# Kernel tuning notes

Hardware: AMD Instinct MI355X
Metric: run time of the kernel (lower is better)

Reference implementation:

```python
import jax, jax.numpy as jnp
import numpy as np
import math

D_MODEL = 1024
N_HEAD = 16


def setup_inputs() -> dict:
    key = jax.random.key(0)
    ks = jax.random.split(key, 5)
    x = jax.random.normal(ks[0], (2, 2048, D_MODEL), dtype=jnp.float32)
    # Linear params (torch Linear: y = x @ W.T + b); store as [in, out] for einsum
    s1 = 1.0 / math.sqrt(D_MODEL)
    W_qkv = jax.random.uniform(ks[1], (D_MODEL, 3 * D_MODEL), jnp.float32, -s1, s1)
    b_qkv = jax.random.uniform(ks[2], (3 * D_MODEL,), jnp.float32, -s1, s1)
    W_out = jax.random.uniform(ks[3], (D_MODEL, D_MODEL), jnp.float32, -s1, s1)
    b_out = jax.random.uniform(ks[4], (D_MODEL,), jnp.float32, -s1, s1)
    return {"x": x, "W_qkv": W_qkv, "b_qkv": b_qkv, "W_out": W_out, "b_out": b_out}


def reference(x, W_qkv, b_qkv, W_out, b_out):
    B, L, D = x.shape
    H = N_HEAD
    hd = D // H
    qkv = x @ W_qkv + b_qkv                      # [B, L, 3D]
    q, k, v = jnp.split(qkv, 3, axis=-1)
    # [B, H, L, hd]
    q = q.reshape(B, L, H, hd).transpose(0, 2, 1, 3)
    k = k.reshape(B, L, H, hd).transpose(0, 2, 1, 3)
    v = v.reshape(B, L, H, hd).transpose(0, 2, 1, 3)
    scale = 1.0 / math.sqrt(hd)
    scores = jnp.einsum('bhqd,bhkd->bhqk', q, k) * scale   # [B, H, L, L]
    causal = jnp.tril(jnp.ones((L, L), dtype=bool))
    scores = jnp.where(causal, scores, jnp.float32(-jnp.inf))
    probs = jax.nn.softmax(scores, axis=-1)
    out = jnp.einsum('bhqk,bhkd->bhqd', probs, v)          # [B, H, L, hd]
    out = out.transpose(0, 2, 1, 3).reshape(B, L, D)
    out = out @ W_out + b_out
    return jnp.squeeze(out)
```

## Files before the change

### kernel.cpp

```cpp
#include <hip/hip_runtime.h>
#include <hip/hip_bf16.h>

#define SEQ    2048
#define NHEAD  16
#define HD     64
#define DMODEL 1024

using bf16 = __hip_bfloat16;
using short8 = __attribute__((ext_vector_type(8))) short;
using short4v = __attribute__((ext_vector_type(4))) short;
using f32x4  = __attribute__((ext_vector_type(4))) float;

__device__ __forceinline__ float fast_exp2(float x) {
  return __builtin_amdgcn_exp2f(x);
}
#define WAIT_LGKM0() __builtin_amdgcn_s_waitcnt(0xC07F)

__device__ __forceinline__ void gload_lds16(const bf16* g, bf16* l) {
  __builtin_amdgcn_global_load_lds(
      (const __attribute__((address_space(1))) void*)g,
      (__attribute__((address_space(3))) void*)l, 16, 0, 0);
}


__global__ void prep_k(const float* __restrict__ x, bf16* __restrict__ xb,
                       const float* __restrict__ Wqkv, bf16* __restrict__ WqkvT,
                       const float* __restrict__ Wout, bf16* __restrict__ WoutT) {
  __shared__ bf16 tile[32][33];
  const int id = blockIdx.x, tid = threadIdx.x;
  if (id < 2048) {
    int i = (id * 256 + tid) * 8;
    bf16 tmp[8];
    #pragma unroll
    for (int j = 0; j < 8; ++j) tmp[j] = __float2bfloat16(x[i + j]);
    *(short8*)&xb[i] = *(short8*)tmp;
    return;
  }
  const float* in; bf16* out; int R, C, tx32, ty32;
  if (id < 2048 + 3072) {
    int t = id - 2048; in = Wqkv; out = WqkvT; R = 1024; C = 3072;
    tx32 = t % 96; ty32 = t / 96;
  } else {
    int t = id - 5120; in = Wout; out = WoutT; R = 1024; C = 1024;
    tx32 = t % 32; ty32 = t / 32;
  }
  int c0 = tx32 * 32, r0 = ty32 * 32;
  int tx = tid & 31, ty = tid >> 5;
  #pragma unroll
  for (int i = ty; i < 32; i += 8)
    tile[i][tx] = __float2bfloat16(in[(size_t)(r0 + i) * C + c0 + tx]);
  __syncthreads();
  #pragma unroll
  for (int i = ty; i < 32; i += 8)
    out[(size_t)(c0 + i) * R + r0 + tx] = tile[tx][i];
}

__global__ void transpose_v_k(const bf16* __restrict__ in, bf16* __restrict__ out) {
  __shared__ bf16 tile[32][33];
  const int bh = blockIdx.z;
  const bf16* ip = in  + (size_t)bh * SEQ * HD;
  bf16* op       = out + (size_t)bh * HD * SEQ;
  int c0 = blockIdx.x * 32, r0 = blockIdx.y * 32;
  int tx = threadIdx.x & 31, ty = threadIdx.x >> 5;
  #pragma unroll
  for (int i = ty; i < 32; i += 8)
    tile[i][tx] = ip[(size_t)(r0 + i) * HD + c0 + tx];
  __syncthreads();
  #pragma unroll
  for (int i = ty; i < 32; i += 8)
    op[(size_t)(c0 + i) * SEQ + r0 + tx] = tile[tx][i];
}

template <int MODE>
__global__ __launch_bounds__(256)
void gemm_bt(const bf16* __restrict__ A, const bf16* __restrict__ BT,
             const float* __restrict__ bias,
             bf16* __restrict__ out0, bf16* __restrict__ out1,
             bf16* __restrict__ out2, float* __restrict__ outf) {
  constexpr int K = 1024;
  __shared__ __align__(16) bf16 As[128 * 32];
  __shared__ __align__(16) bf16 Bs[128 * 32];
  const int tid = threadIdx.x;
  const int wave = tid >> 6, lane = tid & 63;
  const int quad = lane >> 4, l16 = lane & 15;
  const int waveM = (wave >> 1) * 64, waveN = (wave & 1) * 64;
  const int m0 = blockIdx.x * 128, n0 = blockIdx.y * 128;
  const int srow = (lane >> 2);
  const int scol = (((lane & 3) ^ ((lane >> 3) & 3)) * 8);
  const int q8   = (quad ^ ((l16 >> 1) & 3)) * 8;

  const f32x4 zero4 = {0.f, 0.f, 0.f, 0.f};
  f32x4 acc[4][4];
  #pragma unroll
  for (int i = 0; i < 4; ++i)
    #pragma unroll
    for (int j = 0; j < 4; ++j) acc[i][j] = zero4;

  for (int k0 = 0; k0 < K; k0 += 32) {
    __syncthreads();
    #pragma unroll
    for (int half = 0; half < 2; ++half) {
      int grow = half * 64 + wave * 16 + srow;
      gload_lds16(&A [(size_t)(m0 + grow) * K + k0 + scol],
                  &As[(half * 64 + wave * 16) * 32]);
      gload_lds16(&BT[(size_t)(n0 + grow) * K + k0 + scol],
                  &Bs[(half * 64 + wave * 16) * 32]);
    }
    __syncthreads();
    short8 af[4], bfm[4];
    #pragma unroll
    for (int mt = 0; mt < 4; ++mt)
      af[mt] = *(const short8*)&As[(waveM + mt * 16 + l16) * 32 + q8];
    #pragma unroll
    for (int nt = 0; nt < 4; ++nt)
      bfm[nt] = *(const short8*)&Bs[(waveN + nt * 16 + l16) * 32 + q8];
    #pragma unroll
    for (int mt = 0; mt < 4; ++mt)
      #pragma unroll
      for (int nt = 0; nt < 4; ++nt)
        acc[mt][nt] = __builtin_amdgcn_mfma_f32_16x16x32_bf16(
            af[mt], bfm[nt], acc[mt][nt], 0, 0, 0);
  }

  #pragma unroll
  for (int nt = 0; nt < 4; ++nt) {
    int n = n0 + waveN + nt * 16 + l16;
    float bvv = bias[n];
    #pragma unroll
    for (int mt = 0; mt < 4; ++mt) {
      #pragma unroll
      for (int r = 0; r < 4; ++r) {
        int m = m0 + waveM + mt * 16 + quad * 4 + r;
        float v = acc[mt][nt][r] + bvv;
        if (MODE == 1) {
          outf[(size_t)m * 1024 + n] = v;
        } else {
          bf16 v16 = __float2bfloat16(v);
          int which = n >> 10, oo = n & 1023;
          int h = oo >> 6, c = oo & 63;
          int b = m >> 11, l = m & 2047;
          size_t idx = ((size_t)(b * NHEAD + h) * SEQ + l) * HD + c;
          if (which == 0)      out0[idx] = v16;
          else if (which == 1) out1[idx] = v16;
          else                 out2[idx] = v16;
        }
      }
    }
  }
}

__global__ __launch_bounds__(256, 2)
void attn_k(const bf16* __restrict__ Q, const bf16* __restrict__ Kb,
            const bf16* __restrict__ VT, bf16* __restrict__ O) {
  __shared__ __align__(16) bf16 Ks[2][2][64 * 32];
  __shared__ __align__(16) bf16 Vs[2][2][64 * 32];
  __shared__ __align__(16) bf16 Plds[4][2][16][72];
  const int tid = threadIdx.x;
  const int wave = tid >> 6, lane = tid & 63;
  const int quad = lane >> 4, l16 = lane & 15;
  const int srow = lane >> 2;
  const int scol = (((lane & 3) ^ ((lane >> 3) & 3)) * 8);
  const int q8   = (quad ^ ((l16 >> 1) & 3)) * 8;
  const int id = blockIdx.x;
  const int bh = id & 31;
  const int qt = 15 - (id >> 5);
  const int b = bh >> 4, h = bh & 15;

  const bf16* Qp = Q  + (size_t)bh * SEQ * HD;
  const bf16* Kp = Kb + (size_t)bh * SEQ * HD;
  const bf16* Vp = VT + (size_t)bh * HD * SEQ;

  const f32x4 zero4 = {0.f, 0.f, 0.f, 0.f};
  const float c = 0.18033688011112042f;
  const float mc = 8.0f * c;

  const int q0w = qt * 128 + wave * 32;
  const int ntiles = 2 * qt + 2;

  short8 qf[2][2];
  #pragma unroll
  for (int g = 0; g < 2; ++g) {
    qf[g][0] = *(const short8*)&Qp[(size_t)(q0w + g * 16 + l16) * HD + quad * 8];
    qf[g][1] = *(const short8*)&Qp[(size_t)(q0w + g * 16 + l16) * HD + 32 + quad * 8];
  }

  f32x4 oacc[2][4];
  #pragma unroll
  for (int g = 0; g < 2; ++g)
    #pragma unroll
    for (int dt = 0; dt < 4; ++dt) oacc[g][dt] = zero4;
  float l4[2][4] = {{0.f, 0.f, 0.f, 0.f}, {0.f, 0.f, 0.f, 0.f}};

  {
    #pragma unroll
    for (int hh = 0; hh < 2; ++hh)
      gload_lds16(&Kp[(size_t)(wave * 16 + srow) * HD + hh * 32 + scol],
                  &Ks[0][hh][(wave * 16) * 32]);
    #pragma unroll
    for (int ch = 0; ch < 2; ++ch)
      gload_lds16(&Vp[(size_t)(wave * 16 + srow) * SEQ + ch * 32 + scol],
                  &Vs[0][ch][(wave * 16) * 32]);
  }
  __syncthreads();

  for (int t = 0; t < ntiles; ++t) {
    const int buf = t & 1;
    if (t + 1 < ntiles) {
      const int k1 = (t + 1) << 6, nb = buf ^ 1;
      #pragma unroll
      for (int hh = 0; hh < 2; ++hh)
        gload_lds16(&Kp[(size_t)(k1 + wave * 16 + srow) * HD + hh * 32 + scol],
                    &Ks[nb][hh][(wave * 16) * 32]);
      #pragma unroll
      for (int ch = 0; ch < 2; ++ch)
        gload_lds16(&Vp[(size_t)(wave * 16 + srow) * SEQ + k1 + ch * 32 + scol],
                    &Vs[nb][ch][(wave * 16) * 32]);
    }
    const int k0 = t << 6;

    f32x4 s[2][4];
    __builtin_amdgcn_s_setprio(1);
    #pragma unroll
    for (int g4 = 0; g4 < 4; ++g4) {
      short8 ka = *(const short8*)&Ks[buf][0][(g4 * 16 + l16) * 32 + q8];
      short8 kb = *(const short8*)&Ks[buf][1][(g4 * 16 + l16) * 32 + q8];
      #pragma unroll
      for (int g = 0; g < 2; ++g) {
        f32x4 sg = zero4;
        sg = __builtin_amdgcn_mfma_f32_16x16x32_bf16(ka, qf[g][0], sg, 0, 0, 0);
        sg = __builtin_amdgcn_mfma_f32_16x16x32_bf16(kb, qf[g][1], sg, 0, 0, 0);
        s[g][g4] = sg;
      }
    }
    __builtin_amdgcn_s_setprio(0);

    if (t >= ntiles - 2) {
      #pragma unroll
      for (int g = 0; g < 2; ++g) {
        const int q_lane = q0w + g * 16 + l16;
        #pragma unroll
        for (int g4 = 0; g4 < 4; ++g4)
          #pragma unroll
          for (int r = 0; r < 4; ++r) {
            int k = k0 + g4 * 16 + quad * 4 + r;
            s[g][g4][r] = (k <= q_lane) ? s[g][g4][r] : -__builtin_inff();
          }
      }
    }

    #pragma unroll
    for (int g = 0; g < 2; ++g)
      #pragma unroll
      for (int g4 = 0; g4 < 4; ++g4) {
        bf16 pb[4];
        #pragma unroll
        for (int r = 0; r < 4; ++r) {
          float p = fast_exp2(__builtin_fmaf(s[g][g4][r], c, -mc));
          l4[g][r] += p;
          pb[r] = __float2bfloat16(p);
        }
        *(short4v*)&Plds[wave][g][l16][g4 * 16 + quad * 4] = *(short4v*)pb;
      }
    WAIT_LGKM0();

    __builtin_amdgcn_s_setprio(1);
    #pragma unroll
    for (int ch = 0; ch < 2; ++ch) {
      short8 pf0 = *(const short8*)&Plds[wave][0][l16][ch * 32 + quad * 8];
      short8 pf1 = *(const short8*)&Plds[wave][1][l16][ch * 32 + quad * 8];
      #pragma unroll
      for (int dt = 0; dt < 4; ++dt) {
        short8 vf = *(const short8*)&Vs[buf][ch][(dt * 16 + l16) * 32 + q8];
        oacc[0][dt] = __builtin_amdgcn_mfma_f32_16x16x32_bf16(vf, pf0, oacc[0][dt], 0, 0, 0);
        oacc[1][dt] = __builtin_amdgcn_mfma_f32_16x16x32_bf16(vf, pf1, oacc[1][dt], 0, 0, 0);
      }
    }
    __builtin_amdgcn_s_setprio(0);
    __syncthreads();
  }

  #pragma unroll
  for (int g = 0; g < 2; ++g) {
    float l_i = (l4[g][0] + l4[g][1]) + (l4[g][2] + l4[g][3]);
    l_i += __shfl_xor(l_i, 16, 64);
    l_i += __shfl_xor(l_i, 32, 64);
    float inv = 1.f / l_i;
    #pragma unroll
    for (int dt = 0; dt < 4; ++dt) {
      bf16 ob[4];
      #pragma unroll
      for (int r = 0; r < 4; ++r) ob[r] = __float2bfloat16(oacc[g][dt][r] * inv);
      *(short4v*)&Plds[wave][g][l16][dt * 16 + quad * 4] = *(short4v*)ob;
    }
  }
  WAIT_LGKM0();
  {
    int row = lane >> 2;
    int col = (lane & 3) * 16;
    #pragma unroll
    for (int g = 0; g < 2; ++g) {
      short8 o0 = *(const short8*)&Plds[wave][g][row][col];
      short8 o1 = *(const short8*)&Plds[wave][g][row][col + 8];
      size_t base =
          ((size_t)(b * SEQ + q0w + g * 16 + row)) * DMODEL + h * HD + col;
      *(short8*)&O[base]     = o0;
      *(short8*)&O[base + 8] = o1;
    }
  }
}

extern "C" void kernel_launch(void* const* d_in, const int* in_sizes, int n_in,
                              void* d_out, int out_size, void* d_ws, size_t ws_size,
                              hipStream_t stream) {
  const float* x    = (const float*)d_in[0];
  const float* Wqkv = (const float*)d_in[1];
  const float* bqkv = (const float*)d_in[2];
  const float* Wout = (const float*)d_in[3];
  const float* bout = (const float*)d_in[4];
  float* out = (float*)d_out;

  char* ws = (char*)d_ws;
  const size_t MB = 1024 * 1024;
  char* big    = ws + 16384;
  bf16* Kbuf   = (bf16*)(big);
  bf16* VTb    = (bf16*)(big + 8 * MB);
  bf16* xb     = (bf16*)(big + 16 * MB);
  bf16* AO     = (bf16*)(big + 16 * MB);
  bf16* WqkvT  = (bf16*)(big + 24 * MB);
  bf16* WoutT  = (bf16*)(big + 30 * MB);
  bf16* Qb     = (bf16*)d_out;
  bf16* Vtmp   = (bf16*)((char*)d_out + 8 * MB);

  prep_k<<<6144, 256, 0, stream>>>(x, xb, Wqkv, WqkvT, Wout, WoutT);
  gemm_bt<0><<<dim3(4096 / 128, 3072 / 128), 256, 0, stream>>>(
      xb, WqkvT, bqkv, Qb, Kbuf, Vtmp, nullptr);
  transpose_v_k<<<dim3(HD / 32, SEQ / 32, 32), 256, 0, stream>>>(Vtmp, VTb);
  attn_k<<<512, 256, 0, stream>>>(Qb, Kbuf, VTb, AO);
  gemm_bt<1><<<dim3(4096 / 128, 1024 / 128), 256, 0, stream>>>(
      AO, WoutT, bout, nullptr, nullptr, nullptr, out);
}
```

Measured before the change: 186.5 us.

## Use 512-thread attention blocks processing paired causal query tiles

The attention kernel now launches 256 blocks of 8 waves, each covering a 256-row query tile, and each block handles two tiles (pairi and 7-pairi) in sequence so every block does the same total causal work. K and V staging is split across waves, with half loading K and half loading V, and the per-wave P scratch grows to 8 waves. This is meant to remove tail imbalance across CUs and halve K/V reloads per query row. In exchange, blocks are larger and the grid is smaller, so fewer waves may be resident per CU, and more tiles need causal masking.

```diff
diff --git a/kernel.cpp b/kernel.cpp
--- a/kernel.cpp
+++ b/kernel.cpp
@@ -149,12 +149,12 @@
   }
 }
 
-__global__ __launch_bounds__(256, 2)
+__global__ __launch_bounds__(512, 2)
 void attn_k(const bf16* __restrict__ Q, const bf16* __restrict__ Kb,
             const bf16* __restrict__ VT, bf16* __restrict__ O) {
   __shared__ __align__(16) bf16 Ks[2][2][64 * 32];
   __shared__ __align__(16) bf16 Vs[2][2][64 * 32];
-  __shared__ __align__(16) bf16 Plds[4][2][16][72];
+  __shared__ __align__(16) bf16 Plds[8][2][16][72];
   const int tid = threadIdx.x;
   const int wave = tid >> 6, lane = tid & 63;
   const int quad = lane >> 4, l16 = lane & 15;
@@ -163,7 +163,7 @@
   const int q8   = (quad ^ ((l16 >> 1) & 3)) * 8;
   const int id = blockIdx.x;
   const int bh = id & 31;
-  const int qt = 15 - (id >> 5);
+  const int pairi = id >> 5;
   const int b = bh >> 4, h = bh & 15;
 
   const bf16* Qp = Q  + (size_t)bh * SEQ * HD;
@@ -174,138 +174,149 @@
   const float c = 0.18033688011112042f;
   const float mc = 8.0f * c;
 
-  const int q0w = qt * 128 + wave * 32;
-  const int ntiles = 2 * qt + 2;
-
-  short8 qf[2][2];
-  #pragma unroll
-  for (int g = 0; g < 2; ++g) {
-    qf[g][0] = *(const short8*)&Qp[(size_t)(q0w + g * 16 + l16) * HD + quad * 8];
-    qf[g][1] = *(const short8*)&Qp[(size_t)(q0w + g * 16 + l16) * HD + 32 + quad * 8];
-  }
-
-  f32x4 oacc[2][4];
-  #pragma unroll
-  for (int g = 0; g < 2; ++g)
-    #pragma unroll
-    for (int dt = 0; dt < 4; ++dt) oacc[g][dt] = zero4;
-  float l4[2][4] = {{0.f, 0.f, 0.f, 0.f}, {0.f, 0.f, 0.f, 0.f}};
-
-  {
-    #pragma unroll
-    for (int hh = 0; hh < 2; ++hh)
-      gload_lds16(&Kp[(size_t)(wave * 16 + srow) * HD + hh * 32 + scol],
-                  &Ks[0][hh][(wave * 16) * 32]);
-    #pragma unroll
-    for (int ch = 0; ch < 2; ++ch)
-      gload_lds16(&Vp[(size_t)(wave * 16 + srow) * SEQ + ch * 32 + scol],
-                  &Vs[0][ch][(wave * 16) * 32]);
-  }
-  __syncthreads();
-
-  for (int t = 0; t < ntiles; ++t) {
-    const int buf = t & 1;
-    if (t + 1 < ntiles) {
-      const int k1 = (t + 1) << 6, nb = buf ^ 1;
-      #pragma unroll
-      for (int hh = 0; hh < 2; ++hh)
-        gload_lds16(&Kp[(size_t)(k1 + wave * 16 + srow) * HD + hh * 32 + scol],
-                    &Ks[nb][hh][(wave * 16) * 32]);
-      #pragma unroll
-      for (int ch = 0; ch < 2; ++ch)
-        gload_lds16(&Vp[(size_t)(wave * 16 + srow) * SEQ + k1 + ch * 32 + scol],
-                    &Vs[nb][ch][(wave * 16) * 32]);
-    }
-    const int k0 = t << 6;
-
-    f32x4 s[2][4];
-    __builtin_amdgcn_s_setprio(1);
-    #pragma unroll
-    for (int g4 = 0; g4 < 4; ++g4) {
-      short8 ka = *(const short8*)&Ks[buf][0][(g4 * 16 + l16) * 32 + q8];
-      short8 kb = *(const short8*)&Ks[buf][1][(g4 * 16 + l16) * 32 + q8];
-      #pragma unroll
-      for (int g = 0; g < 2; ++g) {
-        f32x4 sg = zero4;
-        sg = __builtin_amdgcn_mfma_f32_16x16x32_bf16(ka, qf[g][0], sg, 0, 0, 0);
-        sg = __builtin_amdgcn_mfma_f32_16x16x32_bf16(kb, qf[g][1], sg, 0, 0, 0);
-        s[g][g4] = sg;
-      }
-    }
-    __builtin_amdgcn_s_setprio(0);
-
-    if (t >= ntiles - 2) {
-      #pragma unroll
-      for (int g = 0; g < 2; ++g) {
-        const int q_lane = q0w + g * 16 + l16;
-        #pragma unroll
-        for (int g4 = 0; g4 < 4; ++g4)
+  const int kslab = (wave & 3) * 16;
+  const bool stK = wave < 4;
+
+  for (int pass = 0; pass < 2; ++pass) {
+    const int qt = pass ? (7 - pairi) : pairi;
+    const int q0w = qt * 256 + wave * 32;
+    const int ntiles = 4 * qt + 4;
+
+    short8 qf[2][2];
+    #pragma unroll
+    for (int g = 0; g < 2; ++g) {
+      qf[g][0] = *(const short8*)&Qp[(size_t)(q0w + g * 16 + l16) * HD + quad * 8];
+      qf[g][1] = *(const short8*)&Qp[(size_t)(q0w + g * 16 + l16) * HD + 32 + quad * 8];
+    }
+
+    f32x4 oacc[2][4];
+    #pragma unroll
+    for (int g = 0; g < 2; ++g)
+      #pragma unroll
+      for (int dt = 0; dt < 4; ++dt) oacc[g][dt] = zero4;
+    float l4[2][4] = {{0.f, 0.f, 0.f, 0.f}, {0.f, 0.f, 0.f, 0.f}};
+
+    if (stK) {
+      gload_lds16(&Kp[(size_t)(kslab + srow) * HD + scol],
+                  &Ks[0][0][kslab * 32]);
+      gload_lds16(&Kp[(size_t)(kslab + srow) * HD + 32 + scol],
+                  &Ks[0][1][kslab * 32]);
+    } else {
+      gload_lds16(&Vp[(size_t)(kslab + srow) * SEQ + scol],
+                  &Vs[0][0][kslab * 32]);
+      gload_lds16(&Vp[(size_t)(kslab + srow) * SEQ + 32 + scol],
+                  &Vs[0][1][kslab * 32]);
+    }
+    __syncthreads();
+
+    for (int t = 0; t < ntiles; ++t) {
+      const int buf = t & 1;
+      if (t + 1 < ntiles) {
+        const int k1 = (t + 1) << 6, nb = buf ^ 1;
+        if (stK) {
+          gload_lds16(&Kp[(size_t)(k1 + kslab + srow) * HD + scol],
+                      &Ks[nb][0][kslab * 32]);
+          gload_lds16(&Kp[(size_t)(k1 + kslab + srow) * HD + 32 + scol],
+                      &Ks[nb][1][kslab * 32]);
+        } else {
+          gload_lds16(&Vp[(size_t)(kslab + srow) * SEQ + k1 + scol],
+                      &Vs[nb][0][kslab * 32]);
+          gload_lds16(&Vp[(size_t)(kslab + srow) * SEQ + k1 + 32 + scol],
+                      &Vs[nb][1][kslab * 32]);
+        }
+      }
+      const int k0 = t << 6;
+
+      f32x4 s[2][4];
+      __builtin_amdgcn_s_setprio(1);
+      #pragma unroll
+      for (int g4 = 0; g4 < 4; ++g4) {
+        short8 ka = *(const short8*)&Ks[buf][0][(g4 * 16 + l16) * 32 + q8];
+        short8 kb = *(const short8*)&Ks[buf][1][(g4 * 16 + l16) * 32 + q8];
+        #pragma unroll
+        for (int g = 0; g < 2; ++g) {
+          f32x4 sg = zero4;
+          sg = __builtin_amdgcn_mfma_f32_16x16x32_bf16(ka, qf[g][0], sg, 0, 0, 0);
+          sg = __builtin_amdgcn_mfma_f32_16x16x32_bf16(kb, qf[g][1], sg, 0, 0, 0);
+          s[g][g4] = sg;
+        }
+      }
+      __builtin_amdgcn_s_setprio(0);
+
+      if (t >= ntiles - 4) {
+        #pragma unroll
+        for (int g = 0; g < 2; ++g) {
+          const int q_lane = q0w + g * 16 + l16;
+          #pragma unroll
+          for (int g4 = 0; g4 < 4; ++g4)
+            #pragma unroll
+            for (int r = 0; r < 4; ++r) {
+              int k = k0 + g4 * 16 + quad * 4 + r;
+              s[g][g4][r] = (k <= q_lane) ? s[g][g4][r] : -__builtin_inff();
+            }
+        }
+      }
+
+      #pragma unroll
+      for (int g = 0; g < 2; ++g)
+        #pragma unroll
+        for (int g4 = 0; g4 < 4; ++g4) {
+          bf16 pb[4];
           #pragma unroll
           for (int r = 0; r < 4; ++r) {
-            int k = k0 + g4 * 16 + quad * 4 + r;
-            s[g][g4][r] = (k <= q_lane) ? s[g][g4][r] : -__builtin_inff();
+            float p = fast_exp2(__builtin_fmaf(s[g][g4][r], c, -mc));
+            l4[g][r] += p;
+            pb[r] = __float2bfloat16(p);
           }
-      }
-    }
-
-    #pragma unroll
-    for (int g = 0; g < 2; ++g)
-      #pragma unroll
-      for (int g4 = 0; g4 < 4; ++g4) {
-        bf16 pb[4];
-        #pragma unroll
-        for (int r = 0; r < 4; ++r) {
-          float p = fast_exp2(__builtin_fmaf(s[g][g4][r], c, -mc));
-          l4[g][r] += p;
-          pb[r] = __float2bfloat16(p);
-        }
-        *(short4v*)&Plds[wave][g][l16][g4 * 16 + quad * 4] = *(short4v*)pb;
-      }
+          *(short4v*)&Plds[wave][g][l16][g4 * 16 + quad * 4] = *(short4v*)pb;
+        }
+      WAIT_LGKM0();
+
+      __builtin_amdgcn_s_setprio(1);
+      #pragma unroll
+      for (int ch = 0; ch < 2; ++ch) {
+        short8 pf0 = *(const short8*)&Plds[wave][0][l16][ch * 32 + quad * 8];
+        short8 pf1 = *(const short8*)&Plds[wave][1][l16][ch * 32 + quad * 8];
+        #pragma unroll
+        for (int dt = 0; dt < 4; ++dt) {
+          short8 vf = *(const short8*)&Vs[buf][ch][(dt * 16 + l16) * 32 + q8];
+          oacc[0][dt] = __builtin_amdgcn_mfma_f32_16x16x32_bf16(vf, pf0, oacc[0][dt], 0, 0, 0);
+          oacc[1][dt] = __builtin_amdgcn_mfma_f32_16x16x32_bf16(vf, pf1, oacc[1][dt], 0, 0, 0);
+        }
+      }
+      __builtin_amdgcn_s_setprio(0);
+      __syncthreads();
+    }
+
+    #pragma unroll
+    for (int g = 0; g < 2; ++g) {
+      float l_i = (l4[g][0] + l4[g][1]) + (l4[g][2] + l4[g][3]);
+      l_i += __shfl_xor(l_i, 16, 64);
+      l_i += __shfl_xor(l_i, 32, 64);
+      float inv = 1.f / l_i;
+      #pragma unroll
+      for (int dt = 0; dt < 4; ++dt) {
+        bf16 ob[4];
+        #pragma unroll
+        for (int r = 0; r < 4; ++r) ob[r] = __float2bfloat16(oacc[g][dt][r] * inv);
+        *(short4v*)&Plds[wave][g][l16][dt * 16 + quad * 4] = *(short4v*)ob;
+      }
+    }
     WAIT_LGKM0();
-
-    __builtin_amdgcn_s_setprio(1);
-    #pragma unroll
-    for (int ch = 0; ch < 2; ++ch) {
-      short8 pf0 = *(const short8*)&Plds[wave][0][l16][ch * 32 + quad * 8];
-      short8 pf1 = *(const short8*)&Plds[wave][1][l16][ch * 32 + quad * 8];
-      #pragma unroll
-      for (int dt = 0; dt < 4; ++dt) {
-        short8 vf = *(const short8*)&Vs[buf][ch][(dt * 16 + l16) * 32 + q8];
-        oacc[0][dt] = __builtin_amdgcn_mfma_f32_16x16x32_bf16(vf, pf0, oacc[0][dt], 0, 0, 0);
-        oacc[1][dt] = __builtin_amdgcn_mfma_f32_16x16x32_bf16(vf, pf1, oacc[1][dt], 0, 0, 0);
-      }
-    }
-    __builtin_amdgcn_s_setprio(0);
-    __syncthreads();
-  }
-
-  #pragma unroll
-  for (int g = 0; g < 2; ++g) {
-    float l_i = (l4[g][0] + l4[g][1]) + (l4[g][2] + l4[g][3]);
-    l_i += __shfl_xor(l_i, 16, 64);
-    l_i += __shfl_xor(l_i, 32, 64);
-    float inv = 1.f / l_i;
-    #pragma unroll
-    for (int dt = 0; dt < 4; ++dt) {
-      bf16 ob[4];
-      #pragma unroll
-      for (int r = 0; r < 4; ++r) ob[r] = __float2bfloat16(oacc[g][dt][r] * inv);
-      *(short4v*)&Plds[wave][g][l16][dt * 16 + quad * 4] = *(short4v*)ob;
-    }
-  }
-  WAIT_LGKM0();
-  {
-    int row = lane >> 2;
-    int col = (lane & 3) * 16;
-    #pragma unroll
-    for (int g = 0; g < 2; ++g) {
-      short8 o0 = *(const short8*)&Plds[wave][g][row][col];
-      short8 o1 = *(const short8*)&Plds[wave][g][row][col + 8];
-      size_t base =
-          ((size_t)(b * SEQ + q0w + g * 16 + row)) * DMODEL + h * HD + col;
-      *(short8*)&O[base]     = o0;
-      *(short8*)&O[base + 8] = o1;
-    }
+    {
+      int row = lane >> 2;
+      int col = (lane & 3) * 16;
+      #pragma unroll
+      for (int g = 0; g < 2; ++g) {
+        short8 o0 = *(const short8*)&Plds[wave][g][row][col];
+        short8 o1 = *(const short8*)&Plds[wave][g][row][col + 8];
+        size_t base =
+            ((size_t)(b * SEQ + q0w + g * 16 + row)) * DMODEL + h * HD + col;
+        *(short8*)&O[base]     = o0;
+        *(short8*)&O[base + 8] = o1;
+      }
+    }
+    WAIT_LGKM0();
   }
 }
 
@@ -335,7 +346,7 @@
   gemm_bt<0><<<dim3(4096 / 128, 3072 / 128), 256, 0, stream>>>(
       xb, WqkvT, bqkv, Qb, Kbuf, Vtmp, nullptr);
   transpose_v_k<<<dim3(HD / 32, SEQ / 32, 32), 256, 0, stream>>>(Vtmp, VTb);
-  attn_k<<<512, 256, 0, stream>>>(Qb, Kbuf, VTb, AO);
+  attn_k<<<256, 512, 0, stream>>>(Qb, Kbuf, VTb, AO);
   gemm_bt<1><<<dim3(4096 / 128, 1024 / 128), 256, 0, stream>>>(
       AO, WoutT, bout, nullptr, nullptr, nullptr, out);
 }
```

After: 199.1 us. +6.7%, slower.
